# Kernel tuning notes

Hardware: AMD Instinct MI355X
Metric: run time of the kernel (lower is better)

The kernel has to match this reference:

```python
import jax, jax.numpy as jnp
import numpy as np
from jax import lax

T = 2048          # tokens (batch*seq, module flattens to [-1, hidden])
H = 2048          # hidden_size
E = 32            # n_routed_experts
DF = 1024         # moe_intermediate_size
DS = 4096         # moe_shared_expert_intermediate_size
TOP_K = 6         # num_experts_per_tok
N_GROUP = 8
TOPK_GROUP = 4
SCALE = 2.5       # routed_scaling_factor
NORM_TOPK = True


def relu2(x):
    r = jax.nn.relu(x)
    return r * r


def setup_inputs() -> dict:
    key = jax.random.key(0)
    ks = jax.random.split(key, 7)
    s = 0.02
    return {
        "x": jax.random.normal(ks[0], (T, H), dtype=jnp.float32),
        "router_w": jax.random.normal(ks[1], (E, H), dtype=jnp.float32) * s,
        "router_b": jax.random.normal(ks[2], (E,), dtype=jnp.float32) * s,
        "w_up": jax.random.normal(ks[3], (E, H, DF), dtype=jnp.float32) * s,
        "w_down": jax.random.normal(ks[4], (E, DF, H), dtype=jnp.float32) * s,
        "shared_up": jax.random.normal(ks[5], (H, DS), dtype=jnp.float32) * s,
        "shared_down": jax.random.normal(ks[6], (DS, H), dtype=jnp.float32) * s,
    }


def _route(x, router_w, router_b):
    # router in fp32: logits -> sigmoid scores -> group-restricted top-k
    logits = x @ router_w.T                                  # [T, E]
    scores = jax.nn.sigmoid(logits)
    sfc = scores + router_b[None, :]                         # scores_for_choice
    gsize = E // N_GROUP
    grp = sfc.reshape(T, N_GROUP, gsize)
    group_scores = lax.top_k(grp, 2)[0].sum(-1)              # [T, n_group] sum of top-2
    _, gidx = lax.top_k(group_scores, TOPK_GROUP)            # [T, topk_group]
    group_mask = jax.nn.one_hot(gidx, N_GROUP, dtype=sfc.dtype).sum(1)  # [T, n_group]
    score_mask = jnp.repeat(group_mask, gsize, axis=1)       # [T, E]
    masked = jnp.where(score_mask > 0, sfc, 0.0)
    _, tidx = lax.top_k(masked, TOP_K)                       # [T, top_k]
    tw = jnp.take_along_axis(scores, tidx, axis=1)           # gather raw scores
    if NORM_TOPK:
        tw = tw / (tw.sum(-1, keepdims=True) + 1e-20)
    tw = tw * SCALE
    return tidx, tw


def reference(x, router_w, router_b, w_up, w_down, shared_up, shared_down):
    tidx, tw = _route(x, router_w, router_b)
    # dense combine weights [T, E]; equals sum of routed weights per expert
    combine = (jax.nn.one_hot(tidx, E, dtype=tw.dtype) * tw[..., None]).sum(1)
    # routed experts (no bias, so scaling before down_proj == scaling the output)
    h = jnp.einsum('td,edf->tef', x, w_up)                   # [T, E, DF]
    a = relu2(h) * combine[:, :, None]
    moe_out = jnp.einsum('tef,efd->td', a, w_down)           # [T, H]
    shared_out = relu2(x @ shared_up) @ shared_down
    return moe_out + shared_out
```

## Files before the change

kernel.cpp:

```cpp
#include <hip/hip_runtime.h>
#include <hip/hip_bf16.h>
#include <math.h>

#define T_TOK 2048
#define HID   2048
#define NE    32
#define DF    1024
#define DSZ   4096
#define TOPK  6
#define NGRP  8
#define TOPKG 4
#define RSCALE 2.5f
#define EXT_E 36
#define NSLOT 20480

typedef __attribute__((ext_vector_type(8))) short short8;
typedef __attribute__((ext_vector_type(4))) float f32x4;

typedef __attribute__((address_space(1))) const void gv1;
typedef __attribute__((address_space(3))) void lv3;

static __device__ __forceinline__ void gload16(const void* g, void* l) {
    __builtin_amdgcn_global_load_lds((gv1*)g, (lv3*)l, 16, 0, 0);
}

static __device__ __forceinline__ unsigned short f2b(float f) {
    union { float f; unsigned u; } v; v.f = f;
    unsigned r = v.u + 0x7fffu + ((v.u >> 16) & 1u);
    return (unsigned short)(r >> 16);
}

static __device__ __forceinline__ float b2f(unsigned short b) {
    union { float f; unsigned u; } v; v.u = ((unsigned)b) << 16;
    return v.f;
}

__global__ __launch_bounds__(256)
void router_kernel(const float* __restrict__ x, const float* __restrict__ rw,
                   const float* __restrict__ rb,
                   int* __restrict__ tidx, float* __restrict__ tw,
                   int* __restrict__ counts, unsigned short* __restrict__ xb) {
    __shared__ float xs[HID];
    __shared__ float part[256];
    __shared__ float scores[NE];
    __shared__ float sfc[NE];
    int t = blockIdx.x;
    int tid = threadIdx.x;
    for (int i = tid; i < HID / 4; i += 256) {
        ((float4*)xs)[i] = ((const float4*)(x + (size_t)t * HID))[i];
    }
    __syncthreads();
    {
        float4 a = ((const float4*)xs)[tid * 2];
        float4 b = ((const float4*)xs)[tid * 2 + 1];
        short8 o;
        o[0] = (short)f2b(a.x); o[1] = (short)f2b(a.y); o[2] = (short)f2b(a.z); o[3] = (short)f2b(a.w);
        o[4] = (short)f2b(b.x); o[5] = (short)f2b(b.y); o[6] = (short)f2b(b.z); o[7] = (short)f2b(b.w);
        *(short8*)(xb + (size_t)t * HID + tid * 8) = o;
    }
    int e = tid & 31, ch = tid >> 5;
    const float* w = rw + (size_t)e * HID + ch * 256;
    const float* xv = xs + ch * 256;
    float p = 0.f;
    #pragma unroll 8
    for (int k = 0; k < 256; ++k) p += xv[k] * w[k];
    part[tid] = p;
    __syncthreads();
    if (tid < 32) {
        float l = 0.f;
        #pragma unroll
        for (int c = 0; c < 8; ++c) l += part[c * 32 + tid];
        float s = 1.f / (1.f + expf(-l));
        scores[tid] = s;
        sfc[tid] = s + rb[tid];
    }
    __syncthreads();
    if (tid == 0) {
        float gs[NGRP];
        for (int g = 0; g < NGRP; ++g) {
            float v[4];
            for (int i = 0; i < 4; ++i) v[i] = sfc[g * 4 + i];
            int bi = 0;
            for (int i = 1; i < 4; ++i) if (v[i] > v[bi]) bi = i;
            float m1 = v[bi]; v[bi] = -INFINITY;
            int bj = 0;
            for (int i = 1; i < 4; ++i) if (v[i] > v[bj]) bj = i;
            gs[g] = m1 + v[bj];
        }
        bool gsel[NGRP];
        for (int g = 0; g < NGRP; ++g) gsel[g] = false;
        for (int k = 0; k < TOPKG; ++k) {
            int bi = -1; float b = -INFINITY;
            for (int g = 0; g < NGRP; ++g)
                if (!gsel[g] && gs[g] > b) { b = gs[g]; bi = g; }
            gsel[bi] = true;
        }
        float masked[NE];
        for (int i = 0; i < NE; ++i) masked[i] = gsel[i >> 2] ? sfc[i] : 0.0f;
        int sel[TOPK]; float wv[TOPK]; float wsum = 0.f;
        for (int k = 0; k < TOPK; ++k) {
            int bi = -1; float b = -INFINITY;
            for (int i = 0; i < NE; ++i)
                if (masked[i] > b) { b = masked[i]; bi = i; }
            masked[bi] = -INFINITY;
            sel[k] = bi; wv[k] = scores[bi]; wsum += wv[k];
        }
        float inv = RSCALE / (wsum + 1e-20f);
        for (int k = 0; k < TOPK; ++k) {
            tidx[t * TOPK + k] = sel[k];
            tw[t * TOPK + k] = wv[k] * inv;
            atomicAdd(&counts[sel[k]], 1);
        }
    }
}

__global__ void scan_kernel(const int* __restrict__ counts, int* __restrict__ offsets) {
    if (threadIdx.x == 0) {
        int a = 0;
        for (int e2 = 0; e2 < NE; ++e2) { offsets[e2] = a; a += counts[e2]; }
        offsets[NE] = a;
        for (int j = 1; j <= 4; ++j) offsets[NE + j] = 12288 + j * T_TOK;
    }
}

__global__ void scatter_kernel(const int* __restrict__ tidx, const float* __restrict__ tw,
                               const int* __restrict__ offsets, int* __restrict__ cursors,
                               int* __restrict__ perm, float* __restrict__ pw,
                               int* __restrict__ slot_of) {
    int t = blockIdx.x * blockDim.x + threadIdx.x;
    if (t >= T_TOK) return;
    for (int k = 0; k < TOPK; ++k) {
        int e = tidx[t * TOPK + k];
        int pos = atomicAdd(&cursors[e], 1);
        int slot = offsets[e] + pos;
        perm[slot] = t;
        pw[slot] = tw[t * TOPK + k];
        slot_of[t * TOPK + k] = slot;
    }
    #pragma unroll
    for (int j = 0; j < 4; ++j) {
        int slot = 12288 + j * T_TOK + t;
        perm[slot] = t;
        pw[slot] = 1.0f;
    }
}

static __device__ __forceinline__ void transpose_tile64(
        const float* __restrict__ src, unsigned short* __restrict__ dst,
        int rs, int Kd, int k0, int n0, char* smem) {
    float (*tl)[65] = (float(*)[65])smem;
    int t = threadIdx.x;
    int r0 = t >> 4;
    int c4 = (t & 15) * 4;
    #pragma unroll
    for (int p = 0; p < 4; ++p) {
        int r = r0 + p * 16;
        float4 v = *(const float4*)(src + (size_t)(k0 + r) * rs + n0 + c4);
        tl[c4 + 0][r] = v.x;
        tl[c4 + 1][r] = v.y;
        tl[c4 + 2][r] = v.z;
        tl[c4 + 3][r] = v.w;
    }
    __syncthreads();
    int n = t >> 2;
    int kq = (t & 3) * 16;
    unsigned short o[16];
    #pragma unroll
    for (int i = 0; i < 16; ++i) o[i] = f2b(tl[n][kq + i]);
    unsigned short* d = dst + (size_t)(n0 + n) * Kd + k0 + kq;
    *(short8*)(d) = *(short8*)&o[0];
    *(short8*)(d + 8) = *(short8*)&o[8];
}

__global__ __launch_bounds__(256)
void transpose_up_kernel(const float* __restrict__ w_up, const float* __restrict__ sh_up,
                         unsigned short* __restrict__ bufU) {
    __shared__ __align__(16) char smem[16640];
    int z = blockIdx.y;
    const float* src; int rs;
    if (z < NE) { src = w_up + (size_t)z * HID * DF; rs = DF; }
    else        { src = sh_up + (size_t)(z - NE) * DF; rs = DSZ; }
    int tile = blockIdx.x;
    int tn = tile & 15, tk = tile >> 4;
    transpose_tile64(src, bufU + (size_t)z * DF * HID, rs, HID, tk * 64, tn * 64, smem);
}

static __device__ void gemm_up_body(int bx, int by, int bz,
                                    const unsigned short* __restrict__ xb,
                                    const unsigned short* __restrict__ bufU,
                                    unsigned short* __restrict__ act,
                                    const int* __restrict__ offsets,
                                    const int* __restrict__ perm,
                                    const float* __restrict__ pw, char* lds) {
    constexpr int K = HID, N = DF;
    char* As = lds;
    char* Bs = lds + 16384;

    int tid = threadIdx.x;
    int lane = tid & 63, wvid = tid >> 6, wr = wvid >> 1, wc = wvid & 1;

    int off = offsets[bz], end = offsets[bz + 1];
    int row0 = off + by * 128;
    if (row0 >= end) return;
    int n0 = bx * 128;

    int lr = lane >> 3;
    int csrc = (((lane & 7) ^ lr) << 4);
    size_t abyte[4], bbyte[4];
    int ldsoff[4];
    const char* Bb = (const char*)bufU + (size_t)bz * ((size_t)N * K * 2);
    #pragma unroll
    for (int p = 0; p < 4; ++p) {
        int r = p * 32 + wvid * 8 + lr;
        int gr = row0 + r;
        if (gr > end - 1) gr = end - 1;
        abyte[p] = (size_t)perm[gr] * (K * 2);
        bbyte[p] = (size_t)(n0 + r) * (K * 2);
        ldsoff[p] = (p * 32 + wvid * 8) * 128;
    }

    f32x4 acc[4][4] = {};
    for (int k0 = 0; k0 < K; k0 += 64) {
        __syncthreads();
        #pragma unroll
        for (int p = 0; p < 4; ++p) {
            gload16((const char*)xb + abyte[p] + k0 * 2 + csrc, As + ldsoff[p]);
            gload16(Bb + bbyte[p] + k0 * 2 + csrc, Bs + ldsoff[p]);
        }
        __syncthreads();
        #pragma unroll
        for (int ks = 0; ks < 2; ++ks) {
            int kg = lane >> 4, r16 = lane & 15;
            short8 af[4], bfr[4];
            #pragma unroll
            for (int m = 0; m < 4; ++m) {
                int r = wr * 64 + m * 16 + r16;
                af[m] = *(const short8*)(As + r * 128 + ((ks * 64 + kg * 16) ^ ((r & 7) << 4)));
            }
            #pragma unroll
            for (int n = 0; n < 4; ++n) {
                int c = wc * 64 + n * 16 + r16;
                bfr[n] = *(const short8*)(Bs + c * 128 + ((ks * 64 + kg * 16) ^ ((c & 7) << 4)));
            }
            #pragma unroll
            for (int m = 0; m < 4; ++m)
                #pragma unroll
                for (int n = 0; n < 4; ++n)
                    acc[m][n] = __builtin_amdgcn_mfma_f32_16x16x32_bf16(af[m], bfr[n], acc[m][n], 0, 0, 0);
        }
    }

    int r16 = lane & 15, rg = lane >> 4;
    #pragma unroll
    for (int m = 0; m < 4; ++m) {
        #pragma unroll
        for (int j = 0; j < 4; ++j) {
            int rr = row0 + wr * 64 + m * 16 + rg * 4 + j;
            if (rr < end) {
                float scale = pw[rr];
                #pragma unroll
                for (int n = 0; n < 4; ++n) {
                    int cc = n0 + wc * 64 + n * 16 + r16;
                    float v = acc[m][n][j];
                    v = v > 0.f ? v * v : 0.f;
                    act[(size_t)rr * N + cc] = f2b(v * scale);
                }
            }
        }
    }
}

__global__ __launch_bounds__(256, 2)
void gemm_up_tdn_kernel(const unsigned short* __restrict__ xb,
                        const unsigned short* __restrict__ bufU,
                        unsigned short* __restrict__ act,
                        const int* __restrict__ offsets, const int* __restrict__ perm,
                        const float* __restrict__ pw,
                        const float* __restrict__ w_dn, const float* __restrict__ sh_dn,
                        unsigned short* __restrict__ bufD) {
    __shared__ __align__(16) char smem[32768];
    int bid = blockIdx.x;
    if (bid % 5 != 0) {
        int tile = bid - bid / 5 - 1;
        int tz = tile >> 9;
        int rem = tile & 511;
        int tn = rem & 31, tk = rem >> 5;
        const float* src = (tz < NE) ? (w_dn + (size_t)tz * DF * HID)
                                     : (sh_dn + (size_t)(tz - NE) * DF * HID);
        transpose_tile64(src, bufD + (size_t)tz * HID * DF, HID, DF, tk * 64, tn * 64, smem);
        return;
    }
    int g = bid / 5;
    gemm_up_body(g & 7, (g >> 3) & 15, g >> 7, xb, bufU, act, offsets, perm, pw, smem);
}

__global__ __launch_bounds__(256, 2)
void gemm_down_kernel(const unsigned short* __restrict__ act, const unsigned short* __restrict__ bufD,
                      unsigned short* __restrict__ slotout, const int* __restrict__ offsets) {
    constexpr int K = DF, N = HID;
    __shared__ __align__(16) char lds[32768];
    char* As = lds;
    char* Bs = lds + 16384;

    int tid = threadIdx.x;
    int lane = tid & 63, wvid = tid >> 6, wr = wvid >> 1, wc = wvid & 1;

    int bz = blockIdx.z;
    int off = offsets[bz], end = offsets[bz + 1];
    int row0 = off + blockIdx.y * 128;
    if (row0 >= end) return;
    int n0 = blockIdx.x * 128;

    int lr = lane >> 3;
    int csrc = (((lane & 7) ^ lr) << 4);
    size_t abyte[4], bbyte[4];
    int ldsoff[4];
    const char* Bb = (const char*)bufD + (size_t)bz * ((size_t)N * K * 2);
    #pragma unroll
    for (int p = 0; p < 4; ++p) {
        int r = p * 32 + wvid * 8 + lr;
        int gr = row0 + r;
        if (gr > end - 1) gr = end - 1;
        abyte[p] = (size_t)gr * (K * 2);
        bbyte[p] = (size_t)(n0 + r) * (K * 2);
        ldsoff[p] = (p * 32 + wvid * 8) * 128;
    }

    f32x4 acc[4][4] = {};
    for (int k0 = 0; k0 < K; k0 += 64) {
        __syncthreads();
        #pragma unroll
        for (int p = 0; p < 4; ++p) {
            gload16((const char*)act + abyte[p] + k0 * 2 + csrc, As + ldsoff[p]);
            gload16(Bb + bbyte[p] + k0 * 2 + csrc, Bs + ldsoff[p]);
        }
        __syncthreads();
        #pragma unroll
        for (int ks = 0; ks < 2; ++ks) {
            int kg = lane >> 4, r16 = lane & 15;
            short8 af[4], bfr[4];
            #pragma unroll
            for (int m = 0; m < 4; ++m) {
                int r = wr * 64 + m * 16 + r16;
                af[m] = *(const short8*)(As + r * 128 + ((ks * 64 + kg * 16) ^ ((r & 7) << 4)));
            }
            #pragma unroll
            for (int n = 0; n < 4; ++n) {
                int c = wc * 64 + n * 16 + r16;
                bfr[n] = *(const short8*)(Bs + c * 128 + ((ks * 64 + kg * 16) ^ ((c & 7) << 4)));
            }
            #pragma unroll
            for (int m = 0; m < 4; ++m)
                #pragma unroll
                for (int n = 0; n < 4; ++n)
                    acc[m][n] = __builtin_amdgcn_mfma_f32_16x16x32_bf16(af[m], bfr[n], acc[m][n], 0, 0, 0);
        }
    }

    int r16 = lane & 15, rg = lane >> 4;
    #pragma unroll
    for (int m = 0; m < 4; ++m) {
        #pragma unroll
        for (int j = 0; j < 4; ++j) {
            int rr = row0 + wr * 64 + m * 16 + rg * 4 + j;
            if (rr < end) {
                #pragma unroll
                for (int n = 0; n < 4; ++n) {
                    int cc = n0 + wc * 64 + n * 16 + r16;
                    slotout[(size_t)rr * N + cc] = f2b(acc[m][n][j]);
                }
            }
        }
    }
}

__global__ void combine_kernel(const unsigned short* __restrict__ slotout,
                               const int* __restrict__ slot_of,
                               float* __restrict__ out) {
    int t = blockIdx.x, tid = threadIdx.x;
    int s[10];
    #pragma unroll
    for (int k = 0; k < TOPK; ++k) s[k] = slot_of[t * TOPK + k];
    #pragma unroll
    for (int j = 0; j < 4; ++j) s[TOPK + j] = 12288 + j * T_TOK + t;
    int c = tid * 8;
    float a[8] = {0.f, 0.f, 0.f, 0.f, 0.f, 0.f, 0.f, 0.f};
    #pragma unroll
    for (int k = 0; k < 10; ++k) {
        short8 v = *(const short8*)(slotout + (size_t)s[k] * HID + c);
        #pragma unroll
        for (int i = 0; i < 8; ++i) a[i] += b2f((unsigned short)v[i]);
    }
    *(float4*)(out + (size_t)t * HID + c) = make_float4(a[0], a[1], a[2], a[3]);
    *(float4*)(out + (size_t)t * HID + c + 4) = make_float4(a[4], a[5], a[6], a[7]);
}

extern "C" void kernel_launch(void* const* d_in, const int* in_sizes, int n_in,
                              void* d_out, int out_size, void* d_ws, size_t ws_size,
                              hipStream_t stream) {
    const float* x     = (const float*)d_in[0];
    const float* rw    = (const float*)d_in[1];
    const float* rb    = (const float*)d_in[2];
    const float* w_up  = (const float*)d_in[3];
    const float* w_dn  = (const float*)d_in[4];
    const float* sh_up = (const float*)d_in[5];
    const float* sh_dn = (const float*)d_in[6];
    float* out = (float*)d_out;
    char* ws = (char*)d_ws;

    int*   counts  = (int*)(ws);
    int*   cursors = (int*)(ws + 128);
    int*   offsets = (int*)(ws + 256);
    int*   tidx    = (int*)(ws + 1024);
    float* tw      = (float*)(ws + 50176);
    int*   slot_of = (int*)(ws + 99328);
    int*   perm    = (int*)(ws + 148480);
    float* pw      = (float*)(ws + 230400);
    unsigned short* xb   = (unsigned short*)(ws + 312320);
    unsigned short* act  = (unsigned short*)(ws + 8700928);
    unsigned short* bufU = (unsigned short*)(ws + 50643968);
    unsigned short* bufD = (unsigned short*)(ws + 201638912);
    unsigned short* slotout = (unsigned short*)(ws + 352633856);

    hipMemsetAsync(ws, 0, 256, stream);

    router_kernel<<<T_TOK, 256, 0, stream>>>(x, rw, rb, tidx, tw, counts, xb);
    scan_kernel<<<1, 64, 0, stream>>>(counts, offsets);
    scatter_kernel<<<(T_TOK + 255) / 256, 256, 0, stream>>>(tidx, tw, offsets, cursors,
                                                            perm, pw, slot_of);

    transpose_up_kernel<<<dim3(512, EXT_E), 256, 0, stream>>>(w_up, sh_up, bufU);

    gemm_up_tdn_kernel<<<23040, 256, 0, stream>>>(xb, bufU, act, offsets, perm, pw,
                                                  w_dn, sh_dn, bufD);

    gemm_down_kernel<<<dim3(HID / 128, T_TOK / 128, EXT_E), 256, 0, stream>>>(
        act, bufD, slotout, offsets);

    combine_kernel<<<T_TOK, 256, 0, stream>>>(slotout, slot_of, out);
}
```

Before: 564.3 us.

## Fuse combine into down GEMM epilogue via float atomic adds to output

The down-projection GEMM now scatters its fp32 results directly into the output rows of the original tokens using atomic adds, indexed through perm. This removes the bf16 slotout buffer, the slot_of bookkeeping and the separate combine kernel. The output is zeroed with a memset first. In exchange there are about 10 atomic adds per output element, which causes contention, and the summation order becomes nondeterministic.

Measured after the change: 618.1 us. 1.1x slower.

```diff
diff --git a/kernel.cpp b/kernel.cpp
--- a/kernel.cpp
+++ b/kernel.cpp
@@ -125,8 +125,7 @@
 
 __global__ void scatter_kernel(const int* __restrict__ tidx, const float* __restrict__ tw,
                                const int* __restrict__ offsets, int* __restrict__ cursors,
-                               int* __restrict__ perm, float* __restrict__ pw,
-                               int* __restrict__ slot_of) {
+                               int* __restrict__ perm, float* __restrict__ pw) {
     int t = blockIdx.x * blockDim.x + threadIdx.x;
     if (t >= T_TOK) return;
     for (int k = 0; k < TOPK; ++k) {
@@ -135,7 +134,6 @@
         int slot = offsets[e] + pos;
         perm[slot] = t;
         pw[slot] = tw[t * TOPK + k];
-        slot_of[t * TOPK + k] = slot;
     }
     #pragma unroll
     for (int j = 0; j < 4; ++j) {
@@ -296,7 +294,8 @@
 
 __global__ __launch_bounds__(256, 2)
 void gemm_down_kernel(const unsigned short* __restrict__ act, const unsigned short* __restrict__ bufD,
-                      unsigned short* __restrict__ slotout, const int* __restrict__ offsets) {
+                      float* __restrict__ out, const int* __restrict__ offsets,
+                      const int* __restrict__ perm) {
     constexpr int K = DF, N = HID;
     __shared__ __align__(16) char lds[32768];
     char* As = lds;
@@ -364,35 +363,15 @@
         for (int j = 0; j < 4; ++j) {
             int rr = row0 + wr * 64 + m * 16 + rg * 4 + j;
             if (rr < end) {
+                int tok = perm[rr];
                 #pragma unroll
                 for (int n = 0; n < 4; ++n) {
                     int cc = n0 + wc * 64 + n * 16 + r16;
-                    slotout[(size_t)rr * N + cc] = f2b(acc[m][n][j]);
+                    unsafeAtomicAdd(&out[(size_t)tok * HID + cc], acc[m][n][j]);
                 }
             }
         }
     }
-}
-
-__global__ void combine_kernel(const unsigned short* __restrict__ slotout,
-                               const int* __restrict__ slot_of,
-                               float* __restrict__ out) {
-    int t = blockIdx.x, tid = threadIdx.x;
-    int s[10];
-    #pragma unroll
-    for (int k = 0; k < TOPK; ++k) s[k] = slot_of[t * TOPK + k];
-    #pragma unroll
-    for (int j = 0; j < 4; ++j) s[TOPK + j] = 12288 + j * T_TOK + t;
-    int c = tid * 8;
-    float a[8] = {0.f, 0.f, 0.f, 0.f, 0.f, 0.f, 0.f, 0.f};
-    #pragma unroll
-    for (int k = 0; k < 10; ++k) {
-        short8 v = *(const short8*)(slotout + (size_t)s[k] * HID + c);
-        #pragma unroll
-        for (int i = 0; i < 8; ++i) a[i] += b2f((unsigned short)v[i]);
-    }
-    *(float4*)(out + (size_t)t * HID + c) = make_float4(a[0], a[1], a[2], a[3]);
-    *(float4*)(out + (size_t)t * HID + c + 4) = make_float4(a[4], a[5], a[6], a[7]);
 }
 
 extern "C" void kernel_launch(void* const* d_in, const int* in_sizes, int n_in,
@@ -413,21 +392,20 @@
     int*   offsets = (int*)(ws + 256);
     int*   tidx    = (int*)(ws + 1024);
     float* tw      = (float*)(ws + 50176);
-    int*   slot_of = (int*)(ws + 99328);
     int*   perm    = (int*)(ws + 148480);
     float* pw      = (float*)(ws + 230400);
     unsigned short* xb   = (unsigned short*)(ws + 312320);
     unsigned short* act  = (unsigned short*)(ws + 8700928);
     unsigned short* bufU = (unsigned short*)(ws + 50643968);
     unsigned short* bufD = (unsigned short*)(ws + 201638912);
-    unsigned short* slotout = (unsigned short*)(ws + 352633856);
 
     hipMemsetAsync(ws, 0, 256, stream);
+    hipMemsetAsync(out, 0, (size_t)out_size * 4, stream);
 
     router_kernel<<<T_TOK, 256, 0, stream>>>(x, rw, rb, tidx, tw, counts, xb);
     scan_kernel<<<1, 64, 0, stream>>>(counts, offsets);
     scatter_kernel<<<(T_TOK + 255) / 256, 256, 0, stream>>>(tidx, tw, offsets, cursors,
-                                                            perm, pw, slot_of);
+                                                            perm, pw);
 
     transpose_up_kernel<<<dim3(512, EXT_E), 256, 0, stream>>>(w_up, sh_up, bufU);
 
@@ -435,7 +413,5 @@
                                                   w_dn, sh_dn, bufD);
 
     gemm_down_kernel<<<dim3(HID / 128, T_TOK / 128, EXT_E), 256, 0, stream>>>(
-        act, bufD, slotout, offsets);
-
-    combine_kernel<<<T_TOK, 256, 0, stream>>>(slotout, slot_of, out);
-}
+        act, bufD, out, offsets, perm);
+}
```

## Split up-weight transpose and overlap its tail with up-GEMM blocks

Applied to the files above, without the earlier changes.

The standalone up-projection weight transpose now converts only the first 12 expert slices up front. A new fused kernel runs up-GEMM blocks for those 12 experts interleaved with transpose tiles for the remaining 24 slices. A second fused kernel runs the up-GEMM for the rest interleaved with the down-weight transpose. The goal is to hide the serial transpose latency behind GEMM work, at the cost of an extra launch and different interleave ratios.

Result: slower. 638.9 us (+13.2%).

```diff
diff --git a/kernel.cpp b/kernel.cpp
--- a/kernel.cpp
+++ b/kernel.cpp
@@ -12,7 +12,7 @@
 #define TOPKG 4
 #define RSCALE 2.5f
 #define EXT_E 36
-#define NSLOT 20480
+#define ZSPLIT 12
 
 typedef __attribute__((ext_vector_type(8))) short short8;
 typedef __attribute__((ext_vector_type(4))) float f32x4;
@@ -172,17 +172,22 @@
     *(short8*)(d + 8) = *(short8*)&o[8];
 }
 
-__global__ __launch_bounds__(256)
-void transpose_up_kernel(const float* __restrict__ w_up, const float* __restrict__ sh_up,
-                         unsigned short* __restrict__ bufU) {
-    __shared__ __align__(16) char smem[16640];
-    int z = blockIdx.y;
+static __device__ __forceinline__ void tu_tile(int z, int tile,
+                                               const float* __restrict__ w_up,
+                                               const float* __restrict__ sh_up,
+                                               unsigned short* __restrict__ bufU, char* smem) {
     const float* src; int rs;
     if (z < NE) { src = w_up + (size_t)z * HID * DF; rs = DF; }
     else        { src = sh_up + (size_t)(z - NE) * DF; rs = DSZ; }
-    int tile = blockIdx.x;
     int tn = tile & 15, tk = tile >> 4;
     transpose_tile64(src, bufU + (size_t)z * DF * HID, rs, HID, tk * 64, tn * 64, smem);
+}
+
+__global__ __launch_bounds__(256)
+void tu_head_kernel(const float* __restrict__ w_up, const float* __restrict__ sh_up,
+                    unsigned short* __restrict__ bufU) {
+    __shared__ __align__(16) char smem[16640];
+    tu_tile(blockIdx.y, blockIdx.x, w_up, sh_up, bufU, smem);
 }
 
 static __device__ void gemm_up_body(int bx, int by, int bz,
@@ -271,17 +276,37 @@
 }
 
 __global__ __launch_bounds__(256, 2)
-void gemm_up_tdn_kernel(const unsigned short* __restrict__ xb,
-                        const unsigned short* __restrict__ bufU,
-                        unsigned short* __restrict__ act,
-                        const int* __restrict__ offsets, const int* __restrict__ perm,
-                        const float* __restrict__ pw,
-                        const float* __restrict__ w_dn, const float* __restrict__ sh_dn,
-                        unsigned short* __restrict__ bufD) {
+void d2_kernel(const unsigned short* __restrict__ xb,
+               const unsigned short* __restrict__ bufU_ro,
+               unsigned short* __restrict__ act,
+               const int* __restrict__ offsets, const int* __restrict__ perm,
+               const float* __restrict__ pw,
+               const float* __restrict__ w_up, const float* __restrict__ sh_up,
+               unsigned short* __restrict__ bufU_wr) {
     __shared__ __align__(16) char smem[32768];
     int bid = blockIdx.x;
-    if (bid % 5 != 0) {
-        int tile = bid - bid / 5 - 1;
+    if (bid % 9 != 0) {
+        int tile = bid - bid / 9 - 1;
+        int tz = ZSPLIT + (tile >> 9);
+        tu_tile(tz, tile & 511, w_up, sh_up, bufU_wr, smem);
+        return;
+    }
+    int g = bid / 9;
+    gemm_up_body(g & 7, (g >> 3) & 15, g >> 7, xb, bufU_ro, act, offsets, perm, pw, smem);
+}
+
+__global__ __launch_bounds__(256, 2)
+void d3_kernel(const unsigned short* __restrict__ xb,
+               const unsigned short* __restrict__ bufU,
+               unsigned short* __restrict__ act,
+               const int* __restrict__ offsets, const int* __restrict__ perm,
+               const float* __restrict__ pw,
+               const float* __restrict__ w_dn, const float* __restrict__ sh_dn,
+               unsigned short* __restrict__ bufD) {
+    __shared__ __align__(16) char smem[32768];
+    int bid = blockIdx.x;
+    if (bid % 7 != 0) {
+        int tile = bid - bid / 7 - 1;
         int tz = tile >> 9;
         int rem = tile & 511;
         int tn = rem & 31, tk = rem >> 5;
@@ -290,8 +315,8 @@
         transpose_tile64(src, bufD + (size_t)tz * HID * DF, HID, DF, tk * 64, tn * 64, smem);
         return;
     }
-    int g = bid / 5;
-    gemm_up_body(g & 7, (g >> 3) & 15, g >> 7, xb, bufU, act, offsets, perm, pw, smem);
+    int g = bid / 7;
+    gemm_up_body(g & 7, (g >> 3) & 15, ZSPLIT + (g >> 7), xb, bufU, act, offsets, perm, pw, smem);
 }
 
 __global__ __launch_bounds__(256, 2)
@@ -429,10 +454,13 @@
     scatter_kernel<<<(T_TOK + 255) / 256, 256, 0, stream>>>(tidx, tw, offsets, cursors,
                                                             perm, pw, slot_of);
 
-    transpose_up_kernel<<<dim3(512, EXT_E), 256, 0, stream>>>(w_up, sh_up, bufU);
-
-    gemm_up_tdn_kernel<<<23040, 256, 0, stream>>>(xb, bufU, act, offsets, perm, pw,
-                                                  w_dn, sh_dn, bufD);
+    tu_head_kernel<<<dim3(512, ZSPLIT), 256, 0, stream>>>(w_up, sh_up, bufU);
+
+    d2_kernel<<<13824, 256, 0, stream>>>(xb, bufU, act, offsets, perm, pw,
+                                         w_up, sh_up, bufU);
+
+    d3_kernel<<<21504, 256, 0, stream>>>(xb, bufU, act, offsets, perm, pw,
+                                         w_dn, sh_dn, bufD);
 
     gemm_down_kernel<<<dim3(HID / 128, T_TOK / 128, EXT_E), 256, 0, stream>>>(
         act, bufD, slotout, offsets);
```
